# Optimization experiments

Hardware: AMD Instinct MI355X
Metric: run time of the kernel (lower is better)

## Reference

```python
import jax, jax.numpy as jnp
import numpy as np
from math import sqrt

BS, SEQ, NV, DM, K = 16, 1024, 512, 256, 8
EPS = 0.05  # sinkhorn epsilon
TEMP = 0.07  # concrete-bernoulli temperature


def setup_inputs() -> dict:
    key = jax.random.key(0)
    k1, k2, k3 = jax.random.split(key, 3)
    x = jax.random.normal(k1, (BS, SEQ, NV), jnp.float32)
    # nn.Linear(seq_len, d_model): weight [d_model, seq_len], bias [d_model]
    W = jax.random.normal(k2, (DM, SEQ), jnp.float32) / sqrt(SEQ)
    b = jnp.zeros((DM,), jnp.float32)
    cluster_emb = jax.random.normal(k3, (K, DM), jnp.float32) / sqrt(DM)
    return {"x": x, "W": W, "b": b, "cluster_emb": cluster_emb}


def _l2norm(z):
    # F.normalize(x, dim=1, p=2) with eps=1e-12 clamp
    n = jnp.maximum(jnp.linalg.norm(z, axis=1, keepdims=True), 1e-12)
    return z / n


def _sinkhorn(q):
    Q = jnp.exp(q / EPS)
    return Q / jnp.sum(Q, axis=1, keepdims=True)


def _concrete_bern(p, key):
    u = jax.random.uniform(key, p.shape, p.dtype, 1e-10, 1.0 - 1e-10)
    noise = jnp.log(u) - jnp.log1p(-u)
    logit = jnp.log(p + 1e-10) - jnp.log(1.0 - p + 1e-10)
    return jax.nn.sigmoid((logit + noise) / TEMP)


def _forward(x, W, b, cluster_emb):
    bs, S, nv = x.shape
    d = W.shape[0]
    k = cluster_emb.shape[0]
    # permute -> [bs, nv, S], Linear(S -> d)
    x_emb = jnp.einsum('bsv,ds->bvd', x, W) + b  # [bs, nv, d]
    x_flat = x_emb.reshape(-1, d)  # [bs*nv, d]
    # cosine-similarity cluster logits
    prob = (_l2norm(x_flat) @ _l2norm(cluster_emb).T).reshape(bs, nv, k)
    prob_temp = _sinkhorn(prob.reshape(-1, k)).reshape(bs, nv, k)  # individual probs
    prob_avg = _sinkhorn(jnp.mean(prob, axis=0))  # [nv, k]
    mask = _concrete_bern(prob_avg, jax.random.key(42))  # [nv, k]
    # CrossAttention with n_heads=1 (dropout inactive in eval)
    scale = 1.0 / sqrt(d)
    scores = jnp.einsum('kd,bvd->bkv', cluster_emb, x_emb)  # [bs, k, nv]
    A = jax.nn.softmax(scale * scores, axis=-1) * mask.T[None]  # masked attn
    V = jnp.einsum('bkv,bvd->bkd', A, x_emb)  # [bs, k, d]
    cluster_emb_avg = jnp.mean(V, axis=0)  # [k, d] (stored attribute in torch)
    # cluster_base_encoding: straight-through bernoulli, broadcast over seq_len
    soft = prob_temp.transpose(2, 0, 1)[..., None]  # [k, bs, nv, 1]
    u = jax.random.uniform(jax.random.key(7), soft.shape, soft.dtype)
    bern = (u < jax.lax.stop_gradient(soft)).astype(soft.dtype)
    extend = jnp.broadcast_to(bern, (k, bs, nv, S))  # [k, bs, nv, S]
    hard = soft + jax.lax.stop_gradient(extend - soft)  # straight-through
    return hard


def reference(x, W, b, cluster_emb):
    return _forward(x, W, b, cluster_emb)
```

## Files before the change

### kernel.cpp

```cpp
#include <hip/hip_runtime.h>
#include <hip/hip_bf16.h>
#include <math.h>
#include <stdint.h>

#define BS 16
#define SEQ 1024
#define NV 512
#define DM 256
#define NK 8

__device__ double g_WC[NK * SEQ];
__device__ double g_Bk[NK];
__device__ double g_nn2p[4 * BS * NV];
__device__ unsigned char g_bits[BS * NV];

__device__ __forceinline__ void threefry2x32_key7(uint32_t x0, uint32_t x1,
                                                  uint32_t& o0, uint32_t& o1) {
    const uint32_t k0 = 0u, k1 = 7u;
    const uint32_t k2 = k0 ^ k1 ^ 0x1BD11BDAu;
    uint32_t v0 = x0 + k0, v1 = x1 + k1;
#define TF_ROUND(r) { v0 += v1; v1 = (v1 << (r)) | (v1 >> (32 - (r))); v1 ^= v0; }
    TF_ROUND(13) TF_ROUND(15) TF_ROUND(26) TF_ROUND(6)
    v0 += k1; v1 += k2 + 1u;
    TF_ROUND(17) TF_ROUND(29) TF_ROUND(16) TF_ROUND(24)
    v0 += k2; v1 += k0 + 2u;
    TF_ROUND(13) TF_ROUND(15) TF_ROUND(26) TF_ROUND(6)
    v0 += k0; v1 += k1 + 3u;
    TF_ROUND(17) TF_ROUND(29) TF_ROUND(16) TF_ROUND(24)
    v0 += k1; v1 += k2 + 4u;
    TF_ROUND(13) TF_ROUND(15) TF_ROUND(26) TF_ROUND(6)
    v0 += k2; v1 += k0 + 5u;
#undef TF_ROUND
    o0 = v0; o1 = v1;
}

__device__ __forceinline__ float bits_to_uniform(uint32_t b) {
    return __uint_as_float((b >> 9) | 0x3F800000u) - 1.0f;
}

__global__ __launch_bounds__(256) void prep_kernel(
        const float* __restrict__ W, const float* __restrict__ bias,
        const float* __restrict__ ce) {
    __shared__ double red[256];
    __shared__ double cen[256];
    const int t = threadIdx.x;
    const int k = blockIdx.x >> 2;
    const int schunk = blockIdx.x & 3;

    double c = (double)ce[k * DM + t];
    red[t] = c * c;
    __syncthreads();
    for (int off = 128; off > 0; off >>= 1) {
        if (t < off) red[t] += red[t + off];
        __syncthreads();
    }
    double nc = fmax(sqrt(red[0]), 1e-12);
    cen[t] = c / nc;
    __syncthreads();
    red[t] = (double)bias[t] * cen[t];
    __syncthreads();
    for (int off = 128; off > 0; off >>= 1) {
        if (t < off) red[t] += red[t + off];
        __syncthreads();
    }
    if (t == 0 && schunk == 0) g_Bk[k] = red[0];

    const int s = schunk * 256 + t;
    double acc = 0.0;
    for (int d = 0; d < DM; ++d)
        acc += cen[d] * (double)W[(size_t)d * SEQ + s];
    g_WC[(size_t)k * SEQ + s] = acc;
}

#define KC 32
__global__ __launch_bounds__(256) void gemm_norm_kernel(
        const float* __restrict__ x, const float* __restrict__ W,
        const float* __restrict__ bias) {
    __shared__ float xs[KC][68];
    __shared__ float wsm[64][33];
    __shared__ double pr[16][64];

    const int t = threadIdx.x;
    const int dblk = blockIdx.x;
    const int vblk = blockIdx.y;
    const int b    = blockIdx.z;
    const int v0 = vblk * 64, d0 = dblk * 64;
    const float* xb = x + (size_t)b * SEQ * NV;

    float acc[4][4];
#pragma unroll
    for (int j = 0; j < 4; ++j)
#pragma unroll
        for (int i = 0; i < 4; ++i) acc[j][i] = 0.0f;

    const int lv  = t & 63, ls4 = t >> 6;
    const int lsw = t & 31, ld8 = t >> 5;
    const int tv4 = (t & 15) * 4, td4 = (t >> 4) * 4;

    for (int s0 = 0; s0 < SEQ; s0 += KC) {
        __syncthreads();
#pragma unroll
        for (int j = 0; j < 8; ++j) {
            int sl = ls4 + 4 * j;
            xs[sl][lv] = xb[(size_t)(s0 + sl) * NV + v0 + lv];
        }
#pragma unroll
        for (int j = 0; j < 8; ++j) {
            int dl = ld8 + 8 * j;
            wsm[dl][lsw] = W[(size_t)(d0 + dl) * SEQ + s0 + lsw];
        }
        __syncthreads();
#pragma unroll
        for (int kk = 0; kk < KC; ++kk) {
            float4 xv = *(const float4*)&xs[kk][tv4];
            float w0 = wsm[td4 + 0][kk];
            float w1 = wsm[td4 + 1][kk];
            float w2 = wsm[td4 + 2][kk];
            float w3 = wsm[td4 + 3][kk];
            acc[0][0] += xv.x * w0; acc[0][1] += xv.x * w1;
            acc[0][2] += xv.x * w2; acc[0][3] += xv.x * w3;
            acc[1][0] += xv.y * w0; acc[1][1] += xv.y * w1;
            acc[1][2] += xv.y * w2; acc[1][3] += xv.y * w3;
            acc[2][0] += xv.z * w0; acc[2][1] += xv.z * w1;
            acc[2][2] += xv.z * w2; acc[2][3] += xv.z * w3;
            acc[3][0] += xv.w * w0; acc[3][1] += xv.w * w1;
            acc[3][2] += xv.w * w2; acc[3][3] += xv.w * w3;
        }
    }

    double p4[4];
#pragma unroll
    for (int j = 0; j < 4; ++j) {
        double s = 0.0;
#pragma unroll
        for (int i = 0; i < 4; ++i) {
            float z = acc[j][i] + bias[d0 + td4 + i];
            double zd = (double)z;
            s += zd * zd;
        }
        p4[j] = s;
    }
    __syncthreads();
#pragma unroll
    for (int j = 0; j < 4; ++j) pr[t >> 4][tv4 + j] = p4[j];
    __syncthreads();
    if (t < 64) {
        double s = 0.0;
#pragma unroll
        for (int r = 0; r < 16; ++r) s += pr[r][t];
        g_nn2p[((size_t)dblk * BS + b) * NV + v0 + t] = s;
    }
}

__global__ __launch_bounds__(256) void prob_bits_kernel(
        const float* __restrict__ x) {
    __shared__ double lds_d[4][64][NK];
    const int t = threadIdx.x;
    const int vblk = blockIdx.x;
    const int b    = blockIdx.y;
    const int v0 = vblk * 64;
    const int vl = t & 63, sc = t >> 6;
    const float* xb = x + (size_t)b * SEQ * NV + v0 + vl;

    double D[NK];
#pragma unroll
    for (int k = 0; k < NK; ++k) D[k] = 0.0;

    const int sbase = sc * 256;
    for (int s = sbase; s < sbase + 256; ++s) {
        double xv = (double)xb[(size_t)s * NV];
#pragma unroll
        for (int k = 0; k < NK; ++k) D[k] += xv * g_WC[(size_t)k * SEQ + s];
    }
#pragma unroll
    for (int k = 0; k < NK; ++k) lds_d[sc][vl][k] = D[k];
    __syncthreads();

    if (t < 64) {
        const int v = v0 + t;
        const int bv = b * NV + v;
        double nn2 = 0.0;
#pragma unroll
        for (int db = 0; db < 4; ++db)
            nn2 += g_nn2p[((size_t)db * BS + b) * NV + v];
        double n = fmax(sqrt(nn2), 1e-12);

        double p[NK], sum = 0.0;
#pragma unroll
        for (int k = 0; k < NK; ++k) {
            double Dk = lds_d[0][t][k] + lds_d[1][t][k] + lds_d[2][t][k] +
                        lds_d[3][t][k] + g_Bk[k];
            double prob = Dk / n;
            p[k] = exp(prob / 0.05);
            sum += p[k];
        }
        unsigned int byte = 0;
#pragma unroll
        for (int k = 0; k < NK; ++k) {
            uint32_t i = (uint32_t)(k * (BS * NV) + bv);
            uint32_t y0, y1;
            threefry2x32_key7(0u, i, y0, y1);
            float u = bits_to_uniform(y0 ^ y1);
            if ((double)u < p[k] / sum) byte |= 1u << k;
        }
        g_bits[bv] = (unsigned char)byte;
    }
}

__global__ __launch_bounds__(256) void write_kernel(float* __restrict__ out) {
    const int t = threadIdx.x;
    const size_t r0 = (size_t)blockIdx.x * 8;
#pragma unroll
    for (int j = 0; j < 8; ++j) {
        size_t r = r0 + j;
        unsigned int bv = (unsigned int)(r & 8191u);
        unsigned int k  = (unsigned int)(r >> 13);
        float v = ((g_bits[bv] >> k) & 1u) ? 1.0f : 0.0f;
        float4 val = make_float4(v, v, v, v);
        ((float4*)(out + r * 1024))[t] = val;
    }
}

extern "C" void kernel_launch(void* const* d_in, const int* in_sizes, int n_in,
                              void* d_out, int out_size, void* d_ws, size_t ws_size,
                              hipStream_t stream) {
    const float* x    = (const float*)d_in[0];
    const float* W    = (const float*)d_in[1];
    const float* bias = (const float*)d_in[2];
    const float* ce   = (const float*)d_in[3];
    float* out = (float*)d_out;

    prep_kernel<<<dim3(32), dim3(256), 0, stream>>>(W, bias, ce);
    gemm_norm_kernel<<<dim3(4, 8, 16), dim3(256), 0, stream>>>(x, W, bias);
    prob_bits_kernel<<<dim3(8, 16), dim3(256), 0, stream>>>(x);
    write_kernel<<<dim3(8192), dim3(256), 0, stream>>>(out);
}
```

Measured before the change: 454.9 us.

## Enlarge GEMM register tiles with split-K, and split the prob reduction across more blocks

The norm GEMM now computes an 8x8 output tile per thread over a 128-wide v tile. Its two thread halves each take half of every K chunk and are then reduced through shared memory, with float4 loads for x and a transposed W layout. The fp64 projection onto the cluster directions is split across 8 sequence chunks into a new partial buffer, with WC staged in LDS. A separate finalize kernel then does the softmax and Bernoulli bits. This targets the low-parallelism prob_bits kernel of only 128 blocks and the GEMM's low arithmetic intensity, at the cost of an extra launch and a global partial buffer.

Measured after the change: 398.7 us. 1.14x faster.

```diff
diff --git a/kernel.cpp b/kernel.cpp
--- a/kernel.cpp
+++ b/kernel.cpp
@@ -12,6 +12,7 @@
 __device__ double g_WC[NK * SEQ];
 __device__ double g_Bk[NK];
 __device__ double g_nn2p[4 * BS * NV];
+__device__ double g_Dp[8 * BS * NV * NK];
 __device__ unsigned char g_bits[BS * NV];
 
 __device__ __forceinline__ void threefry2x32_key7(uint32_t x0, uint32_t x1,
@@ -73,138 +74,183 @@
 }
 
 #define KC 32
+#define XS_LD 132
+#define WS_LD 68
+#define ZS_LD 68
+
 __global__ __launch_bounds__(256) void gemm_norm_kernel(
         const float* __restrict__ x, const float* __restrict__ W,
         const float* __restrict__ bias) {
-    __shared__ float xs[KC][68];
-    __shared__ float wsm[64][33];
-    __shared__ double pr[16][64];
+    __shared__ __align__(16) char smem[43008];
+    float* xs  = (float*)smem;
+    float* wst = (float*)(smem + 16896);
+    float* zS  = (float*)smem;
+    double* pr = (double*)(smem + 34816);
 
     const int t = threadIdx.x;
     const int dblk = blockIdx.x;
     const int vblk = blockIdx.y;
     const int b    = blockIdx.z;
-    const int v0 = vblk * 64, d0 = dblk * 64;
+    const int v0 = vblk * 128, d0 = dblk * 64;
     const float* xb = x + (size_t)b * SEQ * NV;
 
-    float acc[4][4];
-#pragma unroll
-    for (int j = 0; j < 4; ++j)
-#pragma unroll
-        for (int i = 0; i < 4; ++i) acc[j][i] = 0.0f;
-
-    const int lv  = t & 63, ls4 = t >> 6;
-    const int lsw = t & 31, ld8 = t >> 5;
-    const int tv4 = (t & 15) * 4, td4 = (t >> 4) * 4;
+    const int kh  = t >> 7;
+    const int tid = t & 127;
+    const int tv8 = (tid & 15) * 8;
+    const int td8 = (tid >> 4) * 8;
+    const int kb  = kh * 16;
+
+    float acc[8][8];
+#pragma unroll
+    for (int j = 0; j < 8; ++j)
+#pragma unroll
+        for (int i = 0; i < 8; ++i) acc[j][i] = 0.0f;
 
     for (int s0 = 0; s0 < SEQ; s0 += KC) {
         __syncthreads();
 #pragma unroll
+        for (int j = 0; j < 4; ++j) {
+            int lin = j * 256 + t;
+            int sl = lin >> 5;
+            int c4 = (lin & 31) << 2;
+            float4 val = *(const float4*)&xb[(size_t)(s0 + sl) * NV + v0 + c4];
+            *(float4*)&xs[sl * XS_LD + c4] = val;
+        }
+#pragma unroll
         for (int j = 0; j < 8; ++j) {
-            int sl = ls4 + 4 * j;
-            xs[sl][lv] = xb[(size_t)(s0 + sl) * NV + v0 + lv];
-        }
+            int dl = (t >> 5) + 8 * j;
+            int sl = t & 31;
+            wst[sl * WS_LD + dl] = W[(size_t)(d0 + dl) * SEQ + s0 + sl];
+        }
+        __syncthreads();
+#pragma unroll
+        for (int kk = 0; kk < 16; ++kk) {
+            const float* xr = &xs[(kb + kk) * XS_LD + tv8];
+            const float* wr = &wst[(kb + kk) * WS_LD + td8];
+            float4 xv0 = *(const float4*)(xr);
+            float4 xv1 = *(const float4*)(xr + 4);
+            float4 wv0 = *(const float4*)(wr);
+            float4 wv1 = *(const float4*)(wr + 4);
+            float xv[8] = {xv0.x, xv0.y, xv0.z, xv0.w, xv1.x, xv1.y, xv1.z, xv1.w};
+            float wv[8] = {wv0.x, wv0.y, wv0.z, wv0.w, wv1.x, wv1.y, wv1.z, wv1.w};
+#pragma unroll
+            for (int j = 0; j < 8; ++j)
+#pragma unroll
+                for (int i = 0; i < 8; ++i) acc[j][i] += xv[j] * wv[i];
+        }
+    }
+
+    __syncthreads();
+    if (kh == 1) {
 #pragma unroll
         for (int j = 0; j < 8; ++j) {
-            int dl = ld8 + 8 * j;
-            wsm[dl][lsw] = W[(size_t)(d0 + dl) * SEQ + s0 + lsw];
-        }
-        __syncthreads();
-#pragma unroll
-        for (int kk = 0; kk < KC; ++kk) {
-            float4 xv = *(const float4*)&xs[kk][tv4];
-            float w0 = wsm[td4 + 0][kk];
-            float w1 = wsm[td4 + 1][kk];
-            float w2 = wsm[td4 + 2][kk];
-            float w3 = wsm[td4 + 3][kk];
-            acc[0][0] += xv.x * w0; acc[0][1] += xv.x * w1;
-            acc[0][2] += xv.x * w2; acc[0][3] += xv.x * w3;
-            acc[1][0] += xv.y * w0; acc[1][1] += xv.y * w1;
-            acc[1][2] += xv.y * w2; acc[1][3] += xv.y * w3;
-            acc[2][0] += xv.z * w0; acc[2][1] += xv.z * w1;
-            acc[2][2] += xv.z * w2; acc[2][3] += xv.z * w3;
-            acc[3][0] += xv.w * w0; acc[3][1] += xv.w * w1;
-            acc[3][2] += xv.w * w2; acc[3][3] += xv.w * w3;
-        }
-    }
-
-    double p4[4];
-#pragma unroll
-    for (int j = 0; j < 4; ++j) {
+            *(float4*)&zS[(tv8 + j) * ZS_LD + td8]     =
+                make_float4(acc[j][0], acc[j][1], acc[j][2], acc[j][3]);
+            *(float4*)&zS[(tv8 + j) * ZS_LD + td8 + 4] =
+                make_float4(acc[j][4], acc[j][5], acc[j][6], acc[j][7]);
+        }
+    }
+    __syncthreads();
+    if (kh == 0) {
+        double bd[8];
+#pragma unroll
+        for (int i = 0; i < 8; ++i) bd[i] = (double)bias[d0 + td8 + i];
+#pragma unroll
+        for (int j = 0; j < 8; ++j) {
+            double sq = 0.0;
+#pragma unroll
+            for (int i = 0; i < 8; ++i) {
+                double z = (double)acc[j][i] +
+                           (double)zS[(tv8 + j) * ZS_LD + td8 + i] + bd[i];
+                sq += z * z;
+            }
+            pr[(tid >> 4) * 128 + tv8 + j] = sq;
+        }
+    }
+    __syncthreads();
+    if (t < 128) {
         double s = 0.0;
 #pragma unroll
-        for (int i = 0; i < 4; ++i) {
-            float z = acc[j][i] + bias[d0 + td4 + i];
-            double zd = (double)z;
-            s += zd * zd;
-        }
-        p4[j] = s;
-    }
-    __syncthreads();
-#pragma unroll
-    for (int j = 0; j < 4; ++j) pr[t >> 4][tv4 + j] = p4[j];
-    __syncthreads();
-    if (t < 64) {
-        double s = 0.0;
-#pragma unroll
-        for (int r = 0; r < 16; ++r) s += pr[r][t];
+        for (int g = 0; g < 8; ++g) s += pr[g * 128 + t];
         g_nn2p[((size_t)dblk * BS + b) * NV + v0 + t] = s;
     }
 }
 
-__global__ __launch_bounds__(256) void prob_bits_kernel(
-        const float* __restrict__ x) {
-    __shared__ double lds_d[4][64][NK];
+__global__ __launch_bounds__(256) void dkern(const float* __restrict__ x) {
+    __shared__ double wcd[NK][128];
+    __shared__ double dw[4][64][NK];
     const int t = threadIdx.x;
     const int vblk = blockIdx.x;
     const int b    = blockIdx.y;
+    const int sc   = blockIdx.z;
     const int v0 = vblk * 64;
-    const int vl = t & 63, sc = t >> 6;
-    const float* xb = x + (size_t)b * SEQ * NV + v0 + vl;
-
+    const int ss = sc * 128;
+
+#pragma unroll
+    for (int j = 0; j < 4; ++j) {
+        int idx = j * 256 + t;
+        ((double*)wcd)[idx] = g_WC[(size_t)(idx >> 7) * SEQ + ss + (idx & 127)];
+    }
+    __syncthreads();
+
+    const int vl = t & 63, w = t >> 6;
+    const float* xp = x + (size_t)b * SEQ * NV + v0 + vl;
     double D[NK];
 #pragma unroll
     for (int k = 0; k < NK; ++k) D[k] = 0.0;
-
-    const int sbase = sc * 256;
-    for (int s = sbase; s < sbase + 256; ++s) {
-        double xv = (double)xb[(size_t)s * NV];
-#pragma unroll
-        for (int k = 0; k < NK; ++k) D[k] += xv * g_WC[(size_t)k * SEQ + s];
-    }
-#pragma unroll
-    for (int k = 0; k < NK; ++k) lds_d[sc][vl][k] = D[k];
-    __syncthreads();
-
-    if (t < 64) {
-        const int v = v0 + t;
-        const int bv = b * NV + v;
-        double nn2 = 0.0;
-#pragma unroll
-        for (int db = 0; db < 4; ++db)
-            nn2 += g_nn2p[((size_t)db * BS + b) * NV + v];
-        double n = fmax(sqrt(nn2), 1e-12);
-
-        double p[NK], sum = 0.0;
-#pragma unroll
-        for (int k = 0; k < NK; ++k) {
-            double Dk = lds_d[0][t][k] + lds_d[1][t][k] + lds_d[2][t][k] +
-                        lds_d[3][t][k] + g_Bk[k];
-            double prob = Dk / n;
-            p[k] = exp(prob / 0.05);
-            sum += p[k];
-        }
-        unsigned int byte = 0;
-#pragma unroll
-        for (int k = 0; k < NK; ++k) {
-            uint32_t i = (uint32_t)(k * (BS * NV) + bv);
-            uint32_t y0, y1;
-            threefry2x32_key7(0u, i, y0, y1);
-            float u = bits_to_uniform(y0 ^ y1);
-            if ((double)u < p[k] / sum) byte |= 1u << k;
-        }
-        g_bits[bv] = (unsigned char)byte;
-    }
+    const int sw = w * 32;
+    for (int i = 0; i < 32; ++i) {
+        int sl = sw + i;
+        double xv = (double)xp[(size_t)(ss + sl) * NV];
+#pragma unroll
+        for (int k = 0; k < NK; ++k) D[k] += xv * wcd[k][sl];
+    }
+#pragma unroll
+    for (int k = 0; k < NK; ++k) dw[w][vl][k] = D[k];
+    __syncthreads();
+
+    const int v = t & 63, k2 = (t >> 6) * 2;
+#pragma unroll
+    for (int j = 0; j < 2; ++j) {
+        int k = k2 + j;
+        double s = dw[0][v][k] + dw[1][v][k] + dw[2][v][k] + dw[3][v][k];
+        g_Dp[(((size_t)sc * BS + b) * NV + v0 + v) * NK + k] = s;
+    }
+}
+
+__global__ __launch_bounds__(256) void finalize_kernel() {
+    const int bv = blockIdx.x * 256 + threadIdx.x;
+    double nn2 = 0.0;
+#pragma unroll
+    for (int db = 0; db < 4; ++db) nn2 += g_nn2p[(size_t)db * (BS * NV) + bv];
+    double n = fmax(sqrt(nn2), 1e-12);
+
+    double D[NK];
+#pragma unroll
+    for (int k = 0; k < NK; ++k) D[k] = g_Bk[k];
+#pragma unroll
+    for (int sc = 0; sc < 8; ++sc) {
+#pragma unroll
+        for (int k = 0; k < NK; ++k)
+            D[k] += g_Dp[((size_t)sc * (BS * NV) + bv) * NK + k];
+    }
+
+    double p[NK], sum = 0.0;
+#pragma unroll
+    for (int k = 0; k < NK; ++k) {
+        p[k] = exp((D[k] / n) / 0.05);
+        sum += p[k];
+    }
+    unsigned int byte = 0;
+#pragma unroll
+    for (int k = 0; k < NK; ++k) {
+        uint32_t i = (uint32_t)(k * (BS * NV) + bv);
+        uint32_t y0, y1;
+        threefry2x32_key7(0u, i, y0, y1);
+        float u = bits_to_uniform(y0 ^ y1);
+        if ((double)u < p[k] / sum) byte |= 1u << k;
+    }
+    g_bits[bv] = (unsigned char)byte;
 }
 
 __global__ __launch_bounds__(256) void write_kernel(float* __restrict__ out) {
@@ -231,7 +277,8 @@
     float* out = (float*)d_out;
 
     prep_kernel<<<dim3(32), dim3(256), 0, stream>>>(W, bias, ce);
-    gemm_norm_kernel<<<dim3(4, 8, 16), dim3(256), 0, stream>>>(x, W, bias);
-    prob_bits_kernel<<<dim3(8, 16), dim3(256), 0, stream>>>(x);
+    gemm_norm_kernel<<<dim3(4, 4, 16), dim3(256), 0, stream>>>(x, W, bias);
+    dkern<<<dim3(8, 16, 8), dim3(256), 0, stream>>>(x);
+    finalize_kernel<<<dim3(32), dim3(256), 0, stream>>>();
     write_kernel<<<dim3(8192), dim3(256), 0, stream>>>(out);
 }
```
